# Performance work log

Measured on AMD Instinct MI355X. Metric: run time of the kernel, lower is better.

Reference implementation:

```python
import jax, jax.numpy as jnp
import numpy as np

N_TOKENS = 8192
D_MODEL = 1024
D_HIDDEN = 4096
N_EXPERTS = 8
TOP_K = 2


def setup_inputs() -> dict:
    key = jax.random.key(0)
    ks = jax.random.split(key, 7)
    s = 0.02
    return {
        "x": jax.random.normal(ks[0], (N_TOKENS, D_MODEL), dtype=jnp.float32),
        "gate_w": jax.random.normal(ks[1], (D_MODEL, N_EXPERTS), dtype=jnp.float32) * s,
        "gate_b": jnp.zeros((N_EXPERTS,), dtype=jnp.float32),
        "w1": jax.random.normal(ks[2], (N_EXPERTS, D_MODEL, D_HIDDEN), dtype=jnp.float32) * s,
        "b1": jnp.zeros((N_EXPERTS, D_HIDDEN), dtype=jnp.float32),
        "w2": jax.random.normal(ks[3], (N_EXPERTS, D_HIDDEN, D_MODEL), dtype=jnp.float32) * s,
        "b2": jnp.zeros((N_EXPERTS, D_MODEL), dtype=jnp.float32),
    }


def reference(x, gate_w, gate_b, w1, b1, w2, b2):
    # Gating: softmax over experts, then top-k routing
    gate_scores = jax.nn.softmax(x @ gate_w + gate_b, axis=-1)        # [N, E]
    topk_vals, topk_idx = jax.lax.top_k(gate_scores, TOP_K)          # [N, K]

    # Combine weights: sum of topk_vals scattered to expert slots
    onehot = jax.nn.one_hot(topk_idx, N_EXPERTS, dtype=x.dtype)      # [N, K, E]
    combine = jnp.einsum('nk,nke->ne', topk_vals, onehot)            # [N, E]

    # Dense expert evaluation (math identical to masked dispatch: unselected
    # experts receive weight 0 in `combine`).
    h = jax.nn.relu(jnp.einsum('nd,edh->neh', x, w1) + b1)           # [N, E, H]
    expert_out = jnp.einsum('neh,ehd->ned', h, w2) + b2              # [N, E, D]
    output = jnp.einsum('ned,ne->nd', expert_out, combine)           # [N, D]

    # Load-balancing loss from routing counts
    load = jnp.sum(onehot, axis=(0, 1))                              # [E]
    load_balancing_loss = jnp.sum((load / jnp.sum(load)) ** 2)
    return output, load_balancing_loss
```

## Files before the change

kernel.cpp:

```cpp
#include <hip/hip_runtime.h>

#define D_MODEL   1024
#define D_HIDDEN  4096
#define N_EXPERTS 8
#define N_TOKENS  8192
#define NASSIGN   (N_TOKENS * 2)
#define PADCAP    (NASSIGN + N_EXPERTS * 128)
#define ROWT      (PADCAP / 128)

typedef unsigned short u16;
typedef __bf16 bf16x8 __attribute__((ext_vector_type(8)));
typedef float  f32x4  __attribute__((ext_vector_type(4)));

__device__ __forceinline__ u16 f2bf(float f) {
  union { float f; unsigned u; } c; c.f = f;
  unsigned u = c.u;
  u = (u + 0x7fffu + ((u >> 16) & 1u)) >> 16;
  return (u16)u;
}

__device__ __forceinline__ void async16(const void* g, void* l) {
  __builtin_amdgcn_global_load_lds(
      (const __attribute__((address_space(1))) unsigned int*)g,
      (__attribute__((address_space(3))) unsigned int*)l, 16, 0, 0);
}

__global__ __launch_bounds__(64) void gating_kernel(
    const float* __restrict__ x, const float* __restrict__ gw,
    const float* __restrict__ gb, int* __restrict__ counts,
    int* __restrict__ tok_idx, float* __restrict__ tok_w)
{
  const int n = blockIdx.x;
  const int lane = threadIdx.x;
  float acc[8] = {0.f,0.f,0.f,0.f,0.f,0.f,0.f,0.f};
  for (int d = lane; d < D_MODEL; d += 64) {
    float xv = x[(size_t)n * D_MODEL + d];
    const float4* g = (const float4*)&gw[d * 8];
    float4 g0 = g[0], g1 = g[1];
    acc[0] += xv * g0.x; acc[1] += xv * g0.y; acc[2] += xv * g0.z; acc[3] += xv * g0.w;
    acc[4] += xv * g1.x; acc[5] += xv * g1.y; acc[6] += xv * g1.z; acc[7] += xv * g1.w;
  }
  for (int off = 32; off; off >>= 1)
    #pragma unroll
    for (int e = 0; e < 8; ++e) acc[e] += __shfl_xor(acc[e], off, 64);
  if (lane == 0) {
    float l[8], p[8];
    float m = -1e30f;
    for (int e = 0; e < 8; ++e) { l[e] = acc[e] + gb[e]; m = fmaxf(m, l[e]); }
    float s = 0.f;
    for (int e = 0; e < 8; ++e) { p[e] = expf(l[e] - m); s += p[e]; }
    float inv = 1.f / s;
    for (int e = 0; e < 8; ++e) p[e] *= inv;
    int i0 = 0;
    for (int e = 1; e < 8; ++e) if (p[e] > p[i0]) i0 = e;
    int i1 = (i0 == 0) ? 1 : 0;
    for (int e = 0; e < 8; ++e) if (e != i0 && p[e] > p[i1]) i1 = e;
    tok_idx[2 * n]     = i0;  tok_idx[2 * n + 1] = i1;
    tok_w[2 * n]       = p[i0]; tok_w[2 * n + 1] = p[i1];
    atomicAdd(&counts[i0], 1);
    atomicAdd(&counts[i1], 1);
  }
}

__global__ void finalize_routing(const int* __restrict__ counts,
                                 int* __restrict__ offsets,
                                 float* __restrict__ out_loss)
{
  int off = 0;
  for (int e = 0; e < 8; ++e) {
    offsets[e] = off;
    off += ((counts[e] + 127) >> 7) << 7;
  }
  offsets[8] = off;
  float loss = 0.f;
  for (int e = 0; e < 8; ++e) {
    float f = (float)counts[e] * (1.f / (float)NASSIGN);
    loss += f * f;
  }
  *out_loss = loss;
}

__global__ __launch_bounds__(256) void scatter_kernel(
    const int* __restrict__ tok_idx, const float* __restrict__ tok_w,
    const int* __restrict__ offsets, int* __restrict__ cursors,
    int* __restrict__ assign_token, float* __restrict__ assign_w,
    int* __restrict__ tok_pos)
{
  const int n = blockIdx.x * 256 + threadIdx.x;
  #pragma unroll
  for (int k = 0; k < 2; ++k) {
    int e = tok_idx[n * 2 + k];
    int pos = offsets[e] + atomicAdd(&cursors[e], 1);
    assign_token[pos] = n;
    assign_w[pos] = tok_w[n * 2 + k];
    tok_pos[n * 2 + k] = pos;
  }
}

__global__ __launch_bounds__(256) void convert_x_kernel(
    const float* __restrict__ x, u16* __restrict__ xb)
{
  size_t i = ((size_t)blockIdx.x * 256 + threadIdx.x) * 4;
  float4 v = *(const float4*)&x[i];
  unsigned lo = (unsigned)f2bf(v.x) | ((unsigned)f2bf(v.y) << 16);
  unsigned hi = (unsigned)f2bf(v.z) | ((unsigned)f2bf(v.w) << 16);
  uint2 o; o.x = lo; o.y = hi;
  *(uint2*)&xb[i] = o;
}

__global__ __launch_bounds__(256) void transpose_cvt_kernel(
    const float* __restrict__ in, u16* __restrict__ out, int R, int C)
{
  const int e = blockIdx.z;
  const int c0 = blockIdx.x * 32, r0 = blockIdx.y * 32;
  __shared__ float tile[32][33];
  const int tx = threadIdx.x & 31, ty = threadIdx.x >> 5;
  const float* ip = in + (size_t)e * R * C;
  u16* op = out + (size_t)e * R * C;
  #pragma unroll
  for (int i = 0; i < 4; ++i)
    tile[ty + i * 8][tx] = ip[(size_t)(r0 + ty + i * 8) * C + c0 + tx];
  __syncthreads();
  #pragma unroll
  for (int i = 0; i < 4; ++i)
    op[(size_t)(c0 + ty + i * 8) * R + r0 + tx] = f2bf(tile[tx][ty + i * 8]);
}

__global__ __launch_bounds__(256) void gemm1_kernel(
    const u16* __restrict__ xb, const u16* __restrict__ w1t,
    const float* __restrict__ b1, const int* __restrict__ assign_token,
    const int* __restrict__ offsets, u16* __restrict__ hbuf)
{
  const int rt = blockIdx.x, ct = blockIdx.y;
  if (rt * 128 >= offsets[8]) return;
  int e = 0;
  while (offsets[e + 1] <= rt * 128) ++e;

  __shared__ __align__(16) u16 smem[24576];

  const int tid = threadIdx.x;
  const int wave = tid >> 6, lane = tid & 63;

  const int c0 = tid, c1 = tid + 256;
  const int r0 = c0 >> 2, s0 = c0 & 3;
  const int r1 = c1 >> 2, s1 = c1 & 3;
  const int sg0 = s0 ^ ((r0 >> 1) & 3);
  const int sg1 = s1 ^ ((r1 >> 1) & 3);

  const long aBase0 = (long)assign_token[rt * 128 + r0] * D_MODEL + sg0 * 8;
  const long aBase1 = (long)assign_token[rt * 128 + r1] * D_MODEL + sg1 * 8;
  const long bBase0 = ((long)e * D_HIDDEN + ct * 128 + r0) * D_MODEL + sg0 * 8;
  const long bBase1 = ((long)e * D_HIDDEN + ct * 128 + r1) * D_MODEL + sg1 * 8;

  const int wr = (wave >> 1) * 64, wc = (wave & 1) * 64;
  f32x4 acc[4][4];
  #pragma unroll
  for (int i = 0; i < 4; ++i)
    #pragma unroll
    for (int j = 0; j < 4; ++j) acc[i][j] = (f32x4){0.f, 0.f, 0.f, 0.f};

  int aoff[4], boff[4];
  #pragma unroll
  for (int i = 0; i < 4; ++i) {
    int row = wr + i * 16 + (lane & 15);
    aoff[i] = row * 32 + (((lane >> 4) ^ ((row >> 1) & 3)) * 8);
    int rown = wc + i * 16 + (lane & 15);
    boff[i] = rown * 32 + (((lane >> 4) ^ ((rown >> 1) & 3)) * 8);
  }

  #define STAGE1(bi, k0) do { \
    u16* A_ = smem + (bi) * 4096; \
    u16* B_ = smem + 12288 + (bi) * 4096; \
    async16(xb  + aBase0 + (k0), A_ + wave * 512); \
    async16(xb  + aBase1 + (k0), A_ + 2048 + wave * 512); \
    async16(w1t + bBase0 + (k0), B_ + wave * 512); \
    async16(w1t + bBase1 + (k0), B_ + 2048 + wave * 512); \
  } while (0)

  const int NT = D_MODEL / 32;
  STAGE1(0, 0);
  STAGE1(1, 32);
  int bi = 0;
  for (int t = 0; t < NT; ++t) {
    if (t < NT - 1) asm volatile("s_waitcnt vmcnt(4)" ::: "memory");
    else            asm volatile("s_waitcnt vmcnt(0)" ::: "memory");
    __builtin_amdgcn_s_barrier();
    const u16* A = smem + bi * 4096;
    const u16* B = smem + 12288 + bi * 4096;
    bf16x8 a[4], b[4];
    #pragma unroll
    for (int i = 0; i < 4; ++i) a[i] = *(const bf16x8*)&A[aoff[i]];
    #pragma unroll
    for (int j = 0; j < 4; ++j) b[j] = *(const bf16x8*)&B[boff[j]];
    __builtin_amdgcn_s_setprio(1);
    #pragma unroll
    for (int i = 0; i < 4; ++i)
      #pragma unroll
      for (int j = 0; j < 4; ++j)
        acc[i][j] = __builtin_amdgcn_mfma_f32_16x16x32_bf16(a[i], b[j], acc[i][j], 0, 0, 0);
    __builtin_amdgcn_s_setprio(0);
    if (t + 2 < NT) {
      int nb = bi + 2; if (nb >= 3) nb -= 3;
      STAGE1(nb, (t + 2) * 32);
    }
    ++bi; if (bi == 3) bi = 0;
  }
  #undef STAGE1

  float bias[4];
  #pragma unroll
  for (int j = 0; j < 4; ++j)
    bias[j] = b1[(size_t)e * D_HIDDEN + ct * 128 + wc + j * 16 + (lane & 15)];

  __syncthreads();
  u16* Hs = smem;
  #pragma unroll
  for (int i = 0; i < 4; ++i)
    #pragma unroll
    for (int j = 0; j < 4; ++j)
      #pragma unroll
      for (int r = 0; r < 4; ++r) {
        int rl = wr + i * 16 + ((lane >> 4) * 4) + r;
        int cl = wc + j * 16 + (lane & 15);
        Hs[rl * 128 + cl] = f2bf(fmaxf(acc[i][j][r] + bias[j], 0.f));
      }
  __syncthreads();
  #pragma unroll
  for (int t = 0; t < 8; ++t) {
    int cc = tid + t * 256;
    int row = cc >> 4, cs = cc & 15;
    *(uint4*)&hbuf[((size_t)(rt * 128 + row)) * D_HIDDEN + ct * 128 + cs * 8] =
        *(const uint4*)&Hs[row * 128 + cs * 8];
  }
}

template <bool EO>
__global__ __launch_bounds__(256) void gemm2_kernel(
    const u16* __restrict__ hbuf, const u16* __restrict__ w2t,
    const float* __restrict__ b2, const int* __restrict__ assign_token,
    const float* __restrict__ assign_w, const int* __restrict__ offsets,
    float* __restrict__ dst)
{
  const int rt = blockIdx.x, ct = blockIdx.y;
  if (rt * 128 >= offsets[8]) return;
  int e = 0;
  while (offsets[e + 1] <= rt * 128) ++e;

  __shared__ __align__(16) u16 smem[24576];
  __shared__ int tokS[128];
  __shared__ float wS[128];

  const int tid = threadIdx.x;
  const int wave = tid >> 6, lane = tid & 63;
  if (tid < 128) {
    tokS[tid] = assign_token[rt * 128 + tid];
    wS[tid] = assign_w[rt * 128 + tid];
  }

  const int c0 = tid, c1 = tid + 256;
  const int r0 = c0 >> 2, s0 = c0 & 3;
  const int r1 = c1 >> 2, s1 = c1 & 3;
  const int sg0 = s0 ^ ((r0 >> 1) & 3);
  const int sg1 = s1 ^ ((r1 >> 1) & 3);

  const long aBase0 = ((long)(rt * 128 + r0)) * D_HIDDEN + sg0 * 8;
  const long aBase1 = ((long)(rt * 128 + r1)) * D_HIDDEN + sg1 * 8;
  const long bBase0 = ((long)e * D_MODEL + ct * 128 + r0) * D_HIDDEN + sg0 * 8;
  const long bBase1 = ((long)e * D_MODEL + ct * 128 + r1) * D_HIDDEN + sg1 * 8;

  const int wr = (wave >> 1) * 64, wc = (wave & 1) * 64;
  f32x4 acc[4][4];
  #pragma unroll
  for (int i = 0; i < 4; ++i)
    #pragma unroll
    for (int j = 0; j < 4; ++j) acc[i][j] = (f32x4){0.f, 0.f, 0.f, 0.f};

  int aoff[4], boff[4];
  #pragma unroll
  for (int i = 0; i < 4; ++i) {
    int row = wr + i * 16 + (lane & 15);
    aoff[i] = row * 32 + (((lane >> 4) ^ ((row >> 1) & 3)) * 8);
    int rown = wc + i * 16 + (lane & 15);
    boff[i] = rown * 32 + (((lane >> 4) ^ ((rown >> 1) & 3)) * 8);
  }

  #define STAGE2(bi, k0) do { \
    u16* A_ = smem + (bi) * 4096; \
    u16* B_ = smem + 12288 + (bi) * 4096; \
    async16(hbuf + aBase0 + (k0), A_ + wave * 512); \
    async16(hbuf + aBase1 + (k0), A_ + 2048 + wave * 512); \
    async16(w2t  + bBase0 + (k0), B_ + wave * 512); \
    async16(w2t  + bBase1 + (k0), B_ + 2048 + wave * 512); \
  } while (0)

  const int NT = D_HIDDEN / 32;
  STAGE2(0, 0);
  STAGE2(1, 32);
  int bi = 0;
  for (int t = 0; t < NT; ++t) {
    if (t < NT - 1) asm volatile("s_waitcnt vmcnt(4)" ::: "memory");
    else            asm volatile("s_waitcnt vmcnt(0)" ::: "memory");
    __builtin_amdgcn_s_barrier();
    const u16* A = smem + bi * 4096;
    const u16* B = smem + 12288 + bi * 4096;
    bf16x8 a[4], b[4];
    #pragma unroll
    for (int i = 0; i < 4; ++i) a[i] = *(const bf16x8*)&A[aoff[i]];
    #pragma unroll
    for (int j = 0; j < 4; ++j) b[j] = *(const bf16x8*)&B[boff[j]];
    __builtin_amdgcn_s_setprio(1);
    #pragma unroll
    for (int i = 0; i < 4; ++i)
      #pragma unroll
      for (int j = 0; j < 4; ++j)
        acc[i][j] = __builtin_amdgcn_mfma_f32_16x16x32_bf16(a[i], b[j], acc[i][j], 0, 0, 0);
    __builtin_amdgcn_s_setprio(0);
    if (t + 2 < NT) {
      int nb = bi + 2; if (nb >= 3) nb -= 3;
      STAGE2(nb, (t + 2) * 32);
    }
    ++bi; if (bi == 3) bi = 0;
  }
  #undef STAGE2

  float bias[4];
  #pragma unroll
  for (int j = 0; j < 4; ++j)
    bias[j] = b2[(size_t)e * D_MODEL + ct * 128 + wc + j * 16 + (lane & 15)];

  #pragma unroll
  for (int i = 0; i < 4; ++i)
    #pragma unroll
    for (int r = 0; r < 4; ++r) {
      int rl = wr + i * 16 + ((lane >> 4) * 4) + r;
      float wgt = wS[rl];
      if (EO) {
        size_t row = (size_t)(rt * 128 + rl);
        #pragma unroll
        for (int j = 0; j < 4; ++j) {
          float v = (acc[i][j][r] + bias[j]) * wgt;
          dst[row * D_MODEL + ct * 128 + wc + j * 16 + (lane & 15)] = v;
        }
      } else {
        int tok = tokS[rl];
        #pragma unroll
        for (int j = 0; j < 4; ++j) {
          float v = (acc[i][j][r] + bias[j]) * wgt;
          atomicAdd(&dst[(size_t)tok * D_MODEL + ct * 128 + wc + j * 16 + (lane & 15)], v);
        }
      }
    }
}

__global__ __launch_bounds__(256) void combine_kernel(
    const float* __restrict__ eo, const int* __restrict__ tok_pos,
    float* __restrict__ out)
{
  int idx = blockIdx.x * 256 + threadIdx.x;
  int n = idx >> 8;
  int c = (idx & 255) * 4;
  int p0 = tok_pos[2 * n], p1 = tok_pos[2 * n + 1];
  float4 a = *(const float4*)&eo[(size_t)p0 * D_MODEL + c];
  float4 b = *(const float4*)&eo[(size_t)p1 * D_MODEL + c];
  float4 o; o.x = a.x + b.x; o.y = a.y + b.y; o.z = a.z + b.z; o.w = a.w + b.w;
  *(float4*)&out[(size_t)n * D_MODEL + c] = o;
}

__global__ __launch_bounds__(256) void moe_fallback_kernel(
    const float* __restrict__ x, const float* __restrict__ w1,
    const float* __restrict__ b1, const float* __restrict__ w2,
    const float* __restrict__ b2, const int* __restrict__ tok_idx,
    const float* __restrict__ tok_w, float* __restrict__ out)
{
  const int a = blockIdx.x;
  const int n = a >> 1, slot = a & 1;
  const int e = tok_idx[n * 2 + slot];
  const float wgt = tok_w[n * 2 + slot];
  __shared__ float xs[D_MODEL];
  __shared__ float hs[D_HIDDEN];
  const int tid = threadIdx.x;
  for (int d = tid; d < D_MODEL; d += 256) xs[d] = x[(size_t)n * D_MODEL + d];
  __syncthreads();
  for (int h = tid; h < D_HIDDEN; h += 256) {
    float acc = b1[(size_t)e * D_HIDDEN + h];
    for (int d = 0; d < D_MODEL; ++d)
      acc += xs[d] * w1[((size_t)e * D_MODEL + d) * D_HIDDEN + h];
    hs[h] = fmaxf(acc, 0.f);
  }
  __syncthreads();
  for (int d = tid; d < D_MODEL; d += 256) {
    float acc = b2[(size_t)e * D_MODEL + d];
    for (int h = 0; h < D_HIDDEN; ++h)
      acc += hs[h] * w2[((size_t)e * D_HIDDEN + h) * D_MODEL + d];
    atomicAdd(&out[(size_t)n * D_MODEL + d], wgt * acc);
  }
}

extern "C" void kernel_launch(void* const* d_in, const int* in_sizes, int n_in,
                              void* d_out, int out_size, void* d_ws, size_t ws_size,
                              hipStream_t stream) {
  const float* x      = (const float*)d_in[0];
  const float* gate_w = (const float*)d_in[1];
  const float* gate_b = (const float*)d_in[2];
  const float* w1     = (const float*)d_in[3];
  const float* b1     = (const float*)d_in[4];
  const float* w2     = (const float*)d_in[5];
  const float* b2     = (const float*)d_in[6];
  float* out = (float*)d_out;

  char* ws = (char*)d_ws;
  int*   counts       = (int*)(ws + 0);
  int*   cursors      = (int*)(ws + 32);
  int*   offsets      = (int*)(ws + 64);
  int*   tok_idx      = (int*)(ws + 256);
  float* tok_w        = (float*)(ws + 65792);
  int*   tok_pos      = (int*)(ws + 131328);
  int*   assign_token = (int*)(ws + 196864);
  float* assign_w     = (float*)(ws + 266496);
  const size_t X0 = 336128;
  u16* xb   = (u16*)(ws + X0);
  u16* w1t  = (u16*)(ws + X0 + 16777216);
  u16* w2t  = (u16*)(ws + X0);
  u16* hbuf = (u16*)(ws + X0 + 83886080);
  float* eo = (float*)(ws + X0 + 226492416ull);
  const size_t REQ_FAST = X0 + 226492416ull;
  const size_t REQ_EO   = REQ_FAST + 71303168ull;

  const bool fast = (ws_size >= REQ_FAST);
  const bool eoPath = (ws_size >= REQ_EO);

  hipMemsetAsync(ws, 0, fast ? X0 : 336128, stream);
  if (!eoPath) {
    hipMemsetAsync(d_out, 0, (size_t)out_size * sizeof(float), stream);
  }

  gating_kernel<<<N_TOKENS, 64, 0, stream>>>(x, gate_w, gate_b, counts, tok_idx, tok_w);
  finalize_routing<<<1, 1, 0, stream>>>(counts, offsets, out + (out_size - 1));

  if (fast) {
    scatter_kernel<<<N_TOKENS / 256, 256, 0, stream>>>(tok_idx, tok_w, offsets, cursors,
                                                       assign_token, assign_w, tok_pos);
    convert_x_kernel<<<(N_TOKENS * D_MODEL) / 1024, 256, 0, stream>>>(x, xb);
    transpose_cvt_kernel<<<dim3(D_HIDDEN / 32, D_MODEL / 32, N_EXPERTS), 256, 0, stream>>>(
        w1, w1t, D_MODEL, D_HIDDEN);
    gemm1_kernel<<<dim3(ROWT, D_HIDDEN / 128), 256, 0, stream>>>(
        xb, w1t, b1, assign_token, offsets, hbuf);
    transpose_cvt_kernel<<<dim3(D_MODEL / 32, D_HIDDEN / 32, N_EXPERTS), 256, 0, stream>>>(
        w2, w2t, D_HIDDEN, D_MODEL);
    if (eoPath) {
      gemm2_kernel<true><<<dim3(ROWT, D_MODEL / 128), 256, 0, stream>>>(
          hbuf, w2t, b2, assign_token, assign_w, offsets, eo);
      combine_kernel<<<(N_TOKENS * D_MODEL) / 1024, 256, 0, stream>>>(eo, tok_pos, out);
    } else {
      gemm2_kernel<false><<<dim3(ROWT, D_MODEL / 128), 256, 0, stream>>>(
          hbuf, w2t, b2, assign_token, assign_w, offsets, out);
    }
  } else {
    moe_fallback_kernel<<<NASSIGN, 256, 0, stream>>>(x, w1, b1, w2, b2, tok_idx, tok_w, out);
  }
}
```

Before: 858.8 us.

## Widen expert GEMM tiles to 128x256 and pack four tokens per gating block

Both expert GEMMs now compute 128x256 output tiles per block, with each wave holding a 64x128 accumulator (4x8 MFMA tiles). Each A tile loaded into LDS is reused across twice as many output columns, and the grid halves along the column dimension. The cost is 128 accumulator floats per lane, higher register pressure (launch bounds set to 2 waves/EU), more LDS, and fewer blocks for the GPU to schedule. The gating kernel also packs four tokens per 256-thread block to cut the block count.

```diff
diff --git a/kernel.cpp b/kernel.cpp
--- a/kernel.cpp
+++ b/kernel.cpp
@@ -25,13 +25,13 @@
       (__attribute__((address_space(3))) unsigned int*)l, 16, 0, 0);
 }
 
-__global__ __launch_bounds__(64) void gating_kernel(
+__global__ __launch_bounds__(256) void gating_kernel(
     const float* __restrict__ x, const float* __restrict__ gw,
     const float* __restrict__ gb, int* __restrict__ counts,
     int* __restrict__ tok_idx, float* __restrict__ tok_w)
 {
-  const int n = blockIdx.x;
-  const int lane = threadIdx.x;
+  const int n = blockIdx.x * 4 + (threadIdx.x >> 6);
+  const int lane = threadIdx.x & 63;
   float acc[8] = {0.f,0.f,0.f,0.f,0.f,0.f,0.f,0.f};
   for (int d = lane; d < D_MODEL; d += 64) {
     float xv = x[(size_t)n * D_MODEL + d];
@@ -126,7 +126,7 @@
     op[(size_t)(c0 + ty + i * 8) * R + r0 + tx] = f2bf(tile[tx][ty + i * 8]);
 }
 
-__global__ __launch_bounds__(256) void gemm1_kernel(
+__global__ __launch_bounds__(256, 2) void gemm1_kernel(
     const u16* __restrict__ xb, const u16* __restrict__ w1t,
     const float* __restrict__ b1, const int* __restrict__ assign_token,
     const int* __restrict__ offsets, u16* __restrict__ hbuf)
@@ -136,45 +136,58 @@
   int e = 0;
   while (offsets[e + 1] <= rt * 128) ++e;
 
-  __shared__ __align__(16) u16 smem[24576];
+  __shared__ __align__(16) u16 smem[36864];
+  u16* Asm = smem;
+  u16* Bsm = smem + 12288;
 
   const int tid = threadIdx.x;
   const int wave = tid >> 6, lane = tid & 63;
 
-  const int c0 = tid, c1 = tid + 256;
-  const int r0 = c0 >> 2, s0 = c0 & 3;
-  const int r1 = c1 >> 2, s1 = c1 & 3;
-  const int sg0 = s0 ^ ((r0 >> 1) & 3);
-  const int sg1 = s1 ^ ((r1 >> 1) & 3);
-
-  const long aBase0 = (long)assign_token[rt * 128 + r0] * D_MODEL + sg0 * 8;
-  const long aBase1 = (long)assign_token[rt * 128 + r1] * D_MODEL + sg1 * 8;
-  const long bBase0 = ((long)e * D_HIDDEN + ct * 128 + r0) * D_MODEL + sg0 * 8;
-  const long bBase1 = ((long)e * D_HIDDEN + ct * 128 + r1) * D_MODEL + sg1 * 8;
-
-  const int wr = (wave >> 1) * 64, wc = (wave & 1) * 64;
-  f32x4 acc[4][4];
-  #pragma unroll
-  for (int i = 0; i < 4; ++i)
-    #pragma unroll
-    for (int j = 0; j < 4; ++j) acc[i][j] = (f32x4){0.f, 0.f, 0.f, 0.f};
-
-  int aoff[4], boff[4];
+  const int ra0 = tid >> 2,         sa = tid & 3;
+  const int ra1 = (tid + 256) >> 2;
+  const int sga0 = sa ^ ((ra0 >> 1) & 3);
+  const int sga1 = sa ^ ((ra1 >> 1) & 3);
+  const long aBase0 = (long)assign_token[rt * 128 + ra0] * D_MODEL + sga0 * 8;
+  const long aBase1 = (long)assign_token[rt * 128 + ra1] * D_MODEL + sga1 * 8;
+
+  long bBase[4];
+  #pragma unroll
+  for (int k = 0; k < 4; ++k) {
+    int c = tid + k * 256;
+    int r = c >> 2, s = c & 3;
+    int sg = s ^ ((r >> 1) & 3);
+    bBase[k] = ((long)e * D_HIDDEN + ct * 256 + r) * D_MODEL + sg * 8;
+  }
+
+  const int wr = (wave >> 1) * 64;
+  const int wc = (wave & 1) * 128;
+  f32x4 acc[4][8];
+  #pragma unroll
+  for (int i = 0; i < 4; ++i)
+    #pragma unroll
+    for (int j = 0; j < 8; ++j) acc[i][j] = (f32x4){0.f, 0.f, 0.f, 0.f};
+
+  int aoff[4], boff[8];
   #pragma unroll
   for (int i = 0; i < 4; ++i) {
     int row = wr + i * 16 + (lane & 15);
     aoff[i] = row * 32 + (((lane >> 4) ^ ((row >> 1) & 3)) * 8);
-    int rown = wc + i * 16 + (lane & 15);
-    boff[i] = rown * 32 + (((lane >> 4) ^ ((rown >> 1) & 3)) * 8);
+  }
+  #pragma unroll
+  for (int j = 0; j < 8; ++j) {
+    int col = wc + j * 16 + (lane & 15);
+    boff[j] = col * 32 + (((lane >> 4) ^ ((col >> 1) & 3)) * 8);
   }
 
   #define STAGE1(bi, k0) do { \
-    u16* A_ = smem + (bi) * 4096; \
-    u16* B_ = smem + 12288 + (bi) * 4096; \
-    async16(xb  + aBase0 + (k0), A_ + wave * 512); \
-    async16(xb  + aBase1 + (k0), A_ + 2048 + wave * 512); \
-    async16(w1t + bBase0 + (k0), B_ + wave * 512); \
-    async16(w1t + bBase1 + (k0), B_ + 2048 + wave * 512); \
+    u16* A_ = Asm + (bi) * 4096; \
+    u16* B_ = Bsm + (bi) * 8192; \
+    async16(xb  + aBase0   + (k0), A_ + wave * 512); \
+    async16(xb  + aBase1   + (k0), A_ + 2048 + wave * 512); \
+    async16(w1t + bBase[0] + (k0), B_ + wave * 512); \
+    async16(w1t + bBase[1] + (k0), B_ + 2048 + wave * 512); \
+    async16(w1t + bBase[2] + (k0), B_ + 4096 + wave * 512); \
+    async16(w1t + bBase[3] + (k0), B_ + 6144 + wave * 512); \
   } while (0)
 
   const int NT = D_MODEL / 32;
@@ -182,21 +195,21 @@
   STAGE1(1, 32);
   int bi = 0;
   for (int t = 0; t < NT; ++t) {
-    if (t < NT - 1) asm volatile("s_waitcnt vmcnt(4)" ::: "memory");
+    if (t < NT - 1) asm volatile("s_waitcnt vmcnt(6)" ::: "memory");
     else            asm volatile("s_waitcnt vmcnt(0)" ::: "memory");
     __builtin_amdgcn_s_barrier();
-    const u16* A = smem + bi * 4096;
-    const u16* B = smem + 12288 + bi * 4096;
-    bf16x8 a[4], b[4];
+    const u16* A = Asm + bi * 4096;
+    const u16* B = Bsm + bi * 8192;
+    bf16x8 a[4], b[8];
     #pragma unroll
     for (int i = 0; i < 4; ++i) a[i] = *(const bf16x8*)&A[aoff[i]];
     #pragma unroll
-    for (int j = 0; j < 4; ++j) b[j] = *(const bf16x8*)&B[boff[j]];
+    for (int j = 0; j < 8; ++j) b[j] = *(const bf16x8*)&B[boff[j]];
     __builtin_amdgcn_s_setprio(1);
     #pragma unroll
     for (int i = 0; i < 4; ++i)
       #pragma unroll
-      for (int j = 0; j < 4; ++j)
+      for (int j = 0; j < 8; ++j)
         acc[i][j] = __builtin_amdgcn_mfma_f32_16x16x32_bf16(a[i], b[j], acc[i][j], 0, 0, 0);
     __builtin_amdgcn_s_setprio(0);
     if (t + 2 < NT) {
@@ -207,35 +220,35 @@
   }
   #undef STAGE1
 
-  float bias[4];
-  #pragma unroll
-  for (int j = 0; j < 4; ++j)
-    bias[j] = b1[(size_t)e * D_HIDDEN + ct * 128 + wc + j * 16 + (lane & 15)];
+  float bias[8];
+  #pragma unroll
+  for (int j = 0; j < 8; ++j)
+    bias[j] = b1[(size_t)e * D_HIDDEN + ct * 256 + wc + j * 16 + (lane & 15)];
 
   __syncthreads();
   u16* Hs = smem;
   #pragma unroll
   for (int i = 0; i < 4; ++i)
     #pragma unroll
-    for (int j = 0; j < 4; ++j)
+    for (int j = 0; j < 8; ++j)
       #pragma unroll
       for (int r = 0; r < 4; ++r) {
         int rl = wr + i * 16 + ((lane >> 4) * 4) + r;
         int cl = wc + j * 16 + (lane & 15);
-        Hs[rl * 128 + cl] = f2bf(fmaxf(acc[i][j][r] + bias[j], 0.f));
+        Hs[rl * 256 + cl] = f2bf(fmaxf(acc[i][j][r] + bias[j], 0.f));
       }
   __syncthreads();
   #pragma unroll
-  for (int t = 0; t < 8; ++t) {
+  for (int t = 0; t < 16; ++t) {
     int cc = tid + t * 256;
-    int row = cc >> 4, cs = cc & 15;
-    *(uint4*)&hbuf[((size_t)(rt * 128 + row)) * D_HIDDEN + ct * 128 + cs * 8] =
-        *(const uint4*)&Hs[row * 128 + cs * 8];
+    int row = cc >> 5, cs = cc & 31;
+    *(uint4*)&hbuf[((size_t)(rt * 128 + row)) * D_HIDDEN + ct * 256 + cs * 8] =
+        *(const uint4*)&Hs[row * 256 + cs * 8];
   }
 }
 
 template <bool EO>
-__global__ __launch_bounds__(256) void gemm2_kernel(
+__global__ __launch_bounds__(256, 2) void gemm2_kernel(
     const u16* __restrict__ hbuf, const u16* __restrict__ w2t,
     const float* __restrict__ b2, const int* __restrict__ assign_token,
     const float* __restrict__ assign_w, const int* __restrict__ offsets,
@@ -246,7 +259,9 @@
   int e = 0;
   while (offsets[e + 1] <= rt * 128) ++e;
 
-  __shared__ __align__(16) u16 smem[24576];
+  __shared__ __align__(16) u16 smem[36864];
+  u16* Asm = smem;
+  u16* Bsm = smem + 12288;
   __shared__ int tokS[128];
   __shared__ float wS[128];
 
@@ -257,40 +272,51 @@
     wS[tid] = assign_w[rt * 128 + tid];
   }
 
-  const int c0 = tid, c1 = tid + 256;
-  const int r0 = c0 >> 2, s0 = c0 & 3;
-  const int r1 = c1 >> 2, s1 = c1 & 3;
-  const int sg0 = s0 ^ ((r0 >> 1) & 3);
-  const int sg1 = s1 ^ ((r1 >> 1) & 3);
-
-  const long aBase0 = ((long)(rt * 128 + r0)) * D_HIDDEN + sg0 * 8;
-  const long aBase1 = ((long)(rt * 128 + r1)) * D_HIDDEN + sg1 * 8;
-  const long bBase0 = ((long)e * D_MODEL + ct * 128 + r0) * D_HIDDEN + sg0 * 8;
-  const long bBase1 = ((long)e * D_MODEL + ct * 128 + r1) * D_HIDDEN + sg1 * 8;
-
-  const int wr = (wave >> 1) * 64, wc = (wave & 1) * 64;
-  f32x4 acc[4][4];
-  #pragma unroll
-  for (int i = 0; i < 4; ++i)
-    #pragma unroll
-    for (int j = 0; j < 4; ++j) acc[i][j] = (f32x4){0.f, 0.f, 0.f, 0.f};
-
-  int aoff[4], boff[4];
+  const int ra0 = tid >> 2,         sa = tid & 3;
+  const int ra1 = (tid + 256) >> 2;
+  const int sga0 = sa ^ ((ra0 >> 1) & 3);
+  const int sga1 = sa ^ ((ra1 >> 1) & 3);
+  const long aBase0 = ((long)(rt * 128 + ra0)) * D_HIDDEN + sga0 * 8;
+  const long aBase1 = ((long)(rt * 128 + ra1)) * D_HIDDEN + sga1 * 8;
+
+  long bBase[4];
+  #pragma unroll
+  for (int k = 0; k < 4; ++k) {
+    int c = tid + k * 256;
+    int r = c >> 2, s = c & 3;
+    int sg = s ^ ((r >> 1) & 3);
+    bBase[k] = ((long)e * D_MODEL + ct * 256 + r) * D_HIDDEN + sg * 8;
+  }
+
+  const int wr = (wave >> 1) * 64;
+  const int wc = (wave & 1) * 128;
+  f32x4 acc[4][8];
+  #pragma unroll
+  for (int i = 0; i < 4; ++i)
+    #pragma unroll
+    for (int j = 0; j < 8; ++j) acc[i][j] = (f32x4){0.f, 0.f, 0.f, 0.f};
+
+  int aoff[4], boff[8];
   #pragma unroll
   for (int i = 0; i < 4; ++i) {
     int row = wr + i * 16 + (lane & 15);
     aoff[i] = row * 32 + (((lane >> 4) ^ ((row >> 1) & 3)) * 8);
-    int rown = wc + i * 16 + (lane & 15);
-    boff[i] = rown * 32 + (((lane >> 4) ^ ((rown >> 1) & 3)) * 8);
+  }
+  #pragma unroll
+  for (int j = 0; j < 8; ++j) {
+    int col = wc + j * 16 + (lane & 15);
+    boff[j] = col * 32 + (((lane >> 4) ^ ((col >> 1) & 3)) * 8);
   }
 
   #define STAGE2(bi, k0) do { \
-    u16* A_ = smem + (bi) * 4096; \
-    u16* B_ = smem + 12288 + (bi) * 4096; \
-    async16(hbuf + aBase0 + (k0), A_ + wave * 512); \
-    async16(hbuf + aBase1 + (k0), A_ + 2048 + wave * 512); \
-    async16(w2t  + bBase0 + (k0), B_ + wave * 512); \
-    async16(w2t  + bBase1 + (k0), B_ + 2048 + wave * 512); \
+    u16* A_ = Asm + (bi) * 4096; \
+    u16* B_ = Bsm + (bi) * 8192; \
+    async16(hbuf + aBase0   + (k0), A_ + wave * 512); \
+    async16(hbuf + aBase1   + (k0), A_ + 2048 + wave * 512); \
+    async16(w2t  + bBase[0] + (k0), B_ + wave * 512); \
+    async16(w2t  + bBase[1] + (k0), B_ + 2048 + wave * 512); \
+    async16(w2t  + bBase[2] + (k0), B_ + 4096 + wave * 512); \
+    async16(w2t  + bBase[3] + (k0), B_ + 6144 + wave * 512); \
   } while (0)
 
   const int NT = D_HIDDEN / 32;
@@ -298,21 +324,21 @@
   STAGE2(1, 32);
   int bi = 0;
   for (int t = 0; t < NT; ++t) {
-    if (t < NT - 1) asm volatile("s_waitcnt vmcnt(4)" ::: "memory");
+    if (t < NT - 1) asm volatile("s_waitcnt vmcnt(6)" ::: "memory");
     else            asm volatile("s_waitcnt vmcnt(0)" ::: "memory");
     __builtin_amdgcn_s_barrier();
-    const u16* A = smem + bi * 4096;
-    const u16* B = smem + 12288 + bi * 4096;
-    bf16x8 a[4], b[4];
+    const u16* A = Asm + bi * 4096;
+    const u16* B = Bsm + bi * 8192;
+    bf16x8 a[4], b[8];
     #pragma unroll
     for (int i = 0; i < 4; ++i) a[i] = *(const bf16x8*)&A[aoff[i]];
     #pragma unroll
-    for (int j = 0; j < 4; ++j) b[j] = *(const bf16x8*)&B[boff[j]];
+    for (int j = 0; j < 8; ++j) b[j] = *(const bf16x8*)&B[boff[j]];
     __builtin_amdgcn_s_setprio(1);
     #pragma unroll
     for (int i = 0; i < 4; ++i)
       #pragma unroll
-      for (int j = 0; j < 4; ++j)
+      for (int j = 0; j < 8; ++j)
         acc[i][j] = __builtin_amdgcn_mfma_f32_16x16x32_bf16(a[i], b[j], acc[i][j], 0, 0, 0);
     __builtin_amdgcn_s_setprio(0);
     if (t + 2 < NT) {
@@ -323,10 +349,10 @@
   }
   #undef STAGE2
 
-  float bias[4];
-  #pragma unroll
-  for (int j = 0; j < 4; ++j)
-    bias[j] = b2[(size_t)e * D_MODEL + ct * 128 + wc + j * 16 + (lane & 15)];
+  float bias[8];
+  #pragma unroll
+  for (int j = 0; j < 8; ++j)
+    bias[j] = b2[(size_t)e * D_MODEL + ct * 256 + wc + j * 16 + (lane & 15)];
 
   #pragma unroll
   for (int i = 0; i < 4; ++i)
@@ -337,16 +363,16 @@
       if (EO) {
         size_t row = (size_t)(rt * 128 + rl);
         #pragma unroll
-        for (int j = 0; j < 4; ++j) {
+        for (int j = 0; j < 8; ++j) {
           float v = (acc[i][j][r] + bias[j]) * wgt;
-          dst[row * D_MODEL + ct * 128 + wc + j * 16 + (lane & 15)] = v;
+          dst[row * D_MODEL + ct * 256 + wc + j * 16 + (lane & 15)] = v;
         }
       } else {
         int tok = tokS[rl];
         #pragma unroll
-        for (int j = 0; j < 4; ++j) {
+        for (int j = 0; j < 8; ++j) {
           float v = (acc[i][j][r] + bias[j]) * wgt;
-          atomicAdd(&dst[(size_t)tok * D_MODEL + ct * 128 + wc + j * 16 + (lane & 15)], v);
+          atomicAdd(&dst[(size_t)tok * D_MODEL + ct * 256 + wc + j * 16 + (lane & 15)], v);
         }
       }
     }
@@ -434,7 +460,7 @@
     hipMemsetAsync(d_out, 0, (size_t)out_size * sizeof(float), stream);
   }
 
-  gating_kernel<<<N_TOKENS, 64, 0, stream>>>(x, gate_w, gate_b, counts, tok_idx, tok_w);
+  gating_kernel<<<N_TOKENS / 4, 256, 0, stream>>>(x, gate_w, gate_b, counts, tok_idx, tok_w);
   finalize_routing<<<1, 1, 0, stream>>>(counts, offsets, out + (out_size - 1));
 
   if (fast) {
@@ -443,16 +469,16 @@
     convert_x_kernel<<<(N_TOKENS * D_MODEL) / 1024, 256, 0, stream>>>(x, xb);
     transpose_cvt_kernel<<<dim3(D_HIDDEN / 32, D_MODEL / 32, N_EXPERTS), 256, 0, stream>>>(
         w1, w1t, D_MODEL, D_HIDDEN);
-    gemm1_kernel<<<dim3(ROWT, D_HIDDEN / 128), 256, 0, stream>>>(
+    gemm1_kernel<<<dim3(ROWT, D_HIDDEN / 256), 256, 0, stream>>>(
         xb, w1t, b1, assign_token, offsets, hbuf);
     transpose_cvt_kernel<<<dim3(D_MODEL / 32, D_HIDDEN / 32, N_EXPERTS), 256, 0, stream>>>(
         w2, w2t, D_HIDDEN, D_MODEL);
     if (eoPath) {
-      gemm2_kernel<true><<<dim3(ROWT, D_MODEL / 128), 256, 0, stream>>>(
+      gemm2_kernel<true><<<dim3(ROWT, D_MODEL / 256), 256, 0, stream>>>(
           hbuf, w2t, b2, assign_token, assign_w, offsets, eo);
       combine_kernel<<<(N_TOKENS * D_MODEL) / 1024, 256, 0, stream>>>(eo, tok_pos, out);
     } else {
-      gemm2_kernel<false><<<dim3(ROWT, D_MODEL / 128), 256, 0, stream>>>(
+      gemm2_kernel<false><<<dim3(ROWT, D_MODEL / 256), 256, 0, stream>>>(
           hbuf, w2t, b2, assign_token, assign_w, offsets, out);
     }
   } else {
```

Result: faster. 817.4 us (-4.8%).
